# Kernel tuning notes

Measured on AMD Instinct MI355X. Metric: run time of the kernel, lower is better.

## Reference

```python
import jax, jax.numpy as jnp
import numpy as np

GAMMA = 0.96875


def setup_inputs() -> dict:
    key = jax.random.key(0)
    kx, kq, kk, kv = jax.random.split(key, 4)
    B, T, D = 4, 2048, 1024
    x = jax.random.normal(kx, (B, T, D), dtype=jnp.float32)
    Wq = jax.random.normal(kq, (D, D), dtype=jnp.float32) * (1.0 / np.sqrt(D))
    Wk = jax.random.normal(kk, (D, D), dtype=jnp.float32) * (1.0 / np.sqrt(D))
    Wv = jax.random.normal(kv, (D, D), dtype=jnp.float32) * (1.0 / np.sqrt(D))
    return {"x": x, "Wq": Wq, "Wk": Wk, "Wv": Wv}


def reference(x, Wq, Wk, Wv):
    # x: [B, T, D_in]; projections are bias-free Dense layers
    B, T, _ = x.shape
    D = Wq.shape[1]
    Q = jnp.einsum("bti,id->btd", x, Wq)  # [B,T,D]
    K = jnp.einsum("bti,id->btd", x, Wk)
    V = jnp.einsum("bti,id->btd", x, Wv)

    gamma = jnp.asarray(GAMMA, x.dtype)

    # Original: s[t] = gamma*s[t-1] + K[:,t,:]^T @ V[:,t,:]   (a [D,D] state,
    # batch is CONTRACTED by the matmul), then only reduce_sum over the last
    # state axis is used. The recurrence is linear, so it collapses exactly to
    # a [D]-vector recurrence with m_t[d] = sum_b K[b,t,d] * (sum_e V[b,t,e]).
    m = jnp.einsum("btd,bt->td", K, V.sum(axis=-1))  # [T,D]

    def step(s, mt):
        s_new = gamma * s + mt
        return s_new, s_new

    # loop runs t = 1..T-1 starting from s = 0; afterwards s[0] = s[1]
    _, states = jax.lax.scan(step, jnp.zeros((D,), x.dtype), m[1:])  # [T-1,D]
    S = jnp.concatenate([states[:1], states], axis=0)  # [T,D]

    # tf.reshape([T,D] -> [-1, T]) is a row-major element scramble, then transpose
    S = S.reshape(-1, T).T  # [T,D] (scrambled, faithful to the original)

    return S[None, :, :] * Q  # broadcast over batch -> [B,T,D]
```

## Files before the change

kernel.cpp:

```cpp
#include <hip/hip_runtime.h>
#include <hip/hip_bf16.h>
#include <cstddef>

#define T_DIM 2048
#define D_DIM 1024
#define GAMMA_F 0.96875f

typedef __attribute__((ext_vector_type(8))) short bf16x8;
typedef __attribute__((ext_vector_type(8))) ushort ushortx8;
typedef __attribute__((ext_vector_type(4))) float f32x4;

#define AS1 __attribute__((address_space(1)))
#define AS3 __attribute__((address_space(3)))

static __device__ inline ushort f2bs(float f) {
    __hip_bfloat16 h = __float2bfloat16(f);
    return *reinterpret_cast<ushort*>(&h);
}

constexpr float gpw(int n) {
    float r = 1.f;
    for (int i = 0; i < n; ++i) r *= GAMMA_F;
    return r;
}

template <int N>
static __device__ __forceinline__ void vm_wait() {
    static_assert(N == 0 || N == 2 || N == 3 || N == 4 || N == 6 || N == 8,
                  "vm_wait<N>: N not in emitted set");
    if constexpr (N == 0)      asm volatile("s_waitcnt vmcnt(0)" ::: "memory");
    else if constexpr (N == 2) asm volatile("s_waitcnt vmcnt(2)" ::: "memory");
    else if constexpr (N == 3) asm volatile("s_waitcnt vmcnt(3)" ::: "memory");
    else if constexpr (N == 4) asm volatile("s_waitcnt vmcnt(4)" ::: "memory");
    else if constexpr (N == 6) asm volatile("s_waitcnt vmcnt(6)" ::: "memory");
    else if constexpr (N == 8) asm volatile("s_waitcnt vmcnt(8)" ::: "memory");
}
static __device__ __forceinline__ void raw_barrier() {
    asm volatile("s_barrier" ::: "memory");
}
static __device__ __forceinline__ void lgkm0() {
    asm volatile("s_waitcnt lgkmcnt(0)" ::: "memory");
}

__global__ __launch_bounds__(256) void k_prep(const float* __restrict__ Wk,
                                              const float* __restrict__ Wq,
                                              const float* __restrict__ Wv,
                                              ushort* __restrict__ WTk,
                                              ushort* __restrict__ WTq,
                                              float* __restrict__ wv_sum) {
    const int tid = threadIdx.x;
    if (blockIdx.z == 2) {
        __shared__ float red[4];
        const int i = blockIdx.y * 32 + blockIdx.x;
        const float* row = Wv + (size_t)i * D_DIM;
        float p = 0.f;
        for (int c = tid; c < D_DIM; c += 256) p += row[c];
        for (int o = 32; o; o >>= 1) p += __shfl_down(p, o);
        if ((tid & 63) == 0) red[tid >> 6] = p;
        __syncthreads();
        if (tid == 0) wv_sum[i] = red[0] + red[1] + red[2] + red[3];
        return;
    }
    const float* W = (blockIdx.z == 0) ? Wk : Wq;
    ushort* WT     = (blockIdx.z == 0) ? WTk : WTq;
    __shared__ float tile[32][33];
    const int tx = tid & 31, ty = tid >> 5;
    const int kb = blockIdx.x * 32, nb = blockIdx.y * 32;
    #pragma unroll
    for (int r = 0; r < 4; ++r)
        tile[ty + 8 * r][tx] = W[(size_t)(kb + ty + 8 * r) * 1024 + nb + tx];
    __syncthreads();
    #pragma unroll
    for (int r = 0; r < 4; ++r)
        WT[(size_t)(nb + ty + 8 * r) * 1024 + kb + tx] =
            f2bs(tile[tx][ty + 8 * r]);
}

__global__ __launch_bounds__(256) void k_vsum_y(const float* __restrict__ x,
                                                const float* __restrict__ wv_sum,
                                                ushort* __restrict__ yb,
                                                ushort* __restrict__ xb) {
    __shared__ float xs[4][D_DIM];
    __shared__ float red[4][4];
    const int t = blockIdx.x;
    const int tid = threadIdx.x;
    const int lane = tid & 63, wv = tid >> 6;

    #pragma unroll
    for (int b = 0; b < 4; ++b) {
        const float4* xr = (const float4*)(x + ((size_t)b * T_DIM + t) * D_DIM);
        *(float4*)&xs[b][tid * 4] = xr[tid];
    }
    __syncthreads();

    #pragma unroll
    for (int b = 0; b < 4; ++b) {
        float p = 0.f;
        for (int c = tid; c < D_DIM; c += 256) p += xs[b][c] * wv_sum[c];
        for (int o = 32; o; o >>= 1) p += __shfl_down(p, o);
        if (lane == 0) red[wv][b] = p;
    }
    __syncthreads();

    float vs[4];
    #pragma unroll
    for (int b = 0; b < 4; ++b)
        vs[b] = red[0][b] + red[1][b] + red[2][b] + red[3][b];

    if (tid < 128) {
        const int i0 = tid * 8;
        ushortx8 yv;
        #pragma unroll
        for (int j = 0; j < 8; ++j) {
            float a = 0.f;
            #pragma unroll
            for (int b = 0; b < 4; ++b) a += xs[b][i0 + j] * vs[b];
            yv[j] = f2bs(a);
        }
        *(ushortx8*)(yb + (size_t)t * D_DIM + i0) = yv;
    }
    for (int g = tid; g < 512; g += 256) {
        const int b = g >> 7, i0 = (g & 127) * 8;
        ushortx8 xv;
        #pragma unroll
        for (int j = 0; j < 8; ++j) xv[j] = f2bs(xs[b][i0 + j]);
        *(ushortx8*)(xb + ((size_t)b * T_DIM + t) * D_DIM + i0) = xv;
    }
}

template <int MF, int NF, int MODE>
__global__ __launch_bounds__(512, 4) void k_gemm(const ushort* __restrict__ A,
                                                 const ushort* __restrict__ BT,
                                                 float* __restrict__ C,
                                                 const float* __restrict__ S2,
                                                 float* __restrict__ tot) {
    static_assert(MODE != 0 || MF == 2, "fused scan1 requires 32-row wave tiles");
    constexpr int BM = 4 * MF * 16;
    constexpr int BN = 2 * NF * 16;
    constexpr int LOADS = BM / 64 + BN / 64;
    __shared__ ushort As[2][BM][64];
    __shared__ ushort Bs[2][BN][64];
    const int tid = threadIdx.x;
    const int lane = tid & 63, wid = tid >> 6;
    const int wr = wid >> 1, wc = wid & 1;
    const int rowBase = blockIdx.x * BM;
    const int colBase = blockIdx.y * BN;

    f32x4 acc[MF][NF];
    #pragma unroll
    for (int i = 0; i < MF; ++i)
        #pragma unroll
        for (int j = 0; j < NF; ++j) acc[i][j] = f32x4{0.f, 0.f, 0.f, 0.f};

    auto stage = [&](int buf, int kb) {
        #pragma unroll
        for (int q = 0; q < BM / 64; ++q) {
            const int s = q * 8192 + tid * 16;
            const int r = s >> 7, grp = (s >> 4) & 7;
            const int gcol = kb + (((grp ^ (r & 7)) & 7) << 3);
            __builtin_amdgcn_global_load_lds(
                (const AS1 void*)(A + (size_t)(rowBase + r) * 1024 + gcol),
                (AS3 void*)((AS3 char*)&As[buf][0][0] + s), 16, 0, 0);
        }
        #pragma unroll
        for (int q = 0; q < BN / 64; ++q) {
            const int s = q * 8192 + tid * 16;
            const int r = s >> 7, grp = (s >> 4) & 7;
            const int gcol = kb + (((grp ^ (r & 7)) & 7) << 3);
            __builtin_amdgcn_global_load_lds(
                (const AS1 void*)(BT + (size_t)(colBase + r) * 1024 + gcol),
                (AS3 void*)((AS3 char*)&Bs[buf][0][0] + s), 16, 0, 0);
        }
    };

    stage(0, 0);

    #pragma unroll 2
    for (int kt = 0; kt < 16; ++kt) {
        const int cur = kt & 1;
        if (kt < 15) {
            stage(cur ^ 1, (kt + 1) * 64);
            vm_wait<LOADS>();
        } else {
            vm_wait<0>();
        }
        raw_barrier();

        bf16x8 af[2][MF], bfv[2][NF];
        #pragma unroll
        for (int ks = 0; ks < 2; ++ks) {
            const int kg = ks * 4 + (lane >> 4);
            #pragma unroll
            for (int mi = 0; mi < MF; ++mi) {
                const int r = wr * (MF * 16) + mi * 16 + (lane & 15);
                af[ks][mi] = *(const bf16x8*)((const char*)&As[cur][0][0] +
                                              r * 128 + (((kg ^ (r & 7)) & 7) << 4));
            }
            #pragma unroll
            for (int ni = 0; ni < NF; ++ni) {
                const int r = wc * (NF * 16) + ni * 16 + (lane & 15);
                bfv[ks][ni] = *(const bf16x8*)((const char*)&Bs[cur][0][0] +
                                               r * 128 + (((kg ^ (r & 7)) & 7) << 4));
            }
        }
        #pragma unroll
        for (int ks = 0; ks < 2; ++ks)
            #pragma unroll
            for (int mi = 0; mi < MF; ++mi)
                #pragma unroll
                for (int ni = 0; ni < NF; ++ni)
                    acc[mi][ni] = __builtin_amdgcn_mfma_f32_16x16x32_bf16(
                        af[ks][mi], bfv[ks][ni], acc[mi][ni], 0, 0, 0);

        lgkm0();
        raw_barrier();
    }

    #pragma unroll
    for (int mi = 0; mi < MF; ++mi) {
        #pragma unroll
        for (int ni = 0; ni < NF; ++ni) {
            const int col = colBase + wc * (NF * 16) + ni * 16 + (lane & 15);
            #pragma unroll
            for (int q = 0; q < 4; ++q) {
                const int row = rowBase + wr * (MF * 16) + mi * 16 + (lane >> 4) * 4 + q;
                float v = acc[mi][ni][q];
                if (MODE == 1)
                    v *= S2[(size_t)(row & (T_DIM - 1)) * D_DIM + col];
                C[(size_t)row * D_DIM + col] = v;
            }
        }
    }

    if (MODE == 0) {
        const int h = lane >> 4;
        const int t3 = 3 - h;
        const float A0 = ((t3 & 1) ? gpw(4) : 1.f) * ((t3 & 2) ? gpw(8) : 1.f);
        const int chunk = blockIdx.x * 4 + wr;
        #pragma unroll
        for (int ni = 0; ni < NF; ++ni) {
            float part = 0.f;
            #pragma unroll
            for (int mi = 0; mi < MF; ++mi)
                #pragma unroll
                for (int q = 0; q < 4; ++q)
                    part += (A0 * gpw(16 * (MF - 1 - mi) + (3 - q))) * acc[mi][ni][q];
            if (chunk == 0 && h == 0)
                part -= (A0 * gpw(16 * (MF - 1) + 3)) * acc[0][ni][0];
            part += __shfl_xor(part, 16);
            part += __shfl_xor(part, 32);
            if (h == 0) {
                const int col = colBase + wc * (NF * 16) + ni * 16 + (lane & 15);
                tot[(size_t)chunk * D_DIM + col] = part;
            }
        }
    }
}

#define SC_L 32
#define SC_NC 64

__global__ __launch_bounds__(256) void k_scan2(const float* __restrict__ m,
                                               const float* __restrict__ tot,
                                               float* __restrict__ S2) {
    __shared__ float ls[128][65];
    const int tid = threadIdx.x;
    const int cl = tid & 63;
    const int ch = tid >> 6;
    const int col = blockIdx.x * 64 + cl;
    const int chg = blockIdx.y * 4 + ch;
    const int t0 = chg * SC_L;

    constexpr float gL = gpw(SC_L);

    float carry = 0.f, f = 1.f;
    for (int j = chg - 1; j >= 0; --j) {
        carry += f * tot[(size_t)j * D_DIM + col];
        f *= gL;
    }

    float r = carry, s1 = 0.f;
    #pragma unroll 4
    for (int k = 0; k < SC_L; ++k) {
        const int t = t0 + k;
        const float a = (t == 0) ? 0.f : m[(size_t)t * D_DIM + col];
        r = GAMMA_F * r + a;
        ls[ch * SC_L + k][cl] = r;
        if (t == 1) s1 = r;
    }
    if (blockIdx.y == 0 && ch == 0) ls[0][cl] = s1;
    __syncthreads();

    const int c0 = blockIdx.x * 64;
    const int tB = blockIdx.y * 128;
    for (int e = tid; e < 128 * 64; e += 256) {
        const int rr = e >> 6;
        const int j  = e & 63;
        const int hi = rr >> 6, cl2 = rr & 63;
        S2[(size_t)((hi << 10) + c0 + cl2) * D_DIM + (tB >> 1) + j] =
            ls[2 * j + hi][cl2];
    }
}

extern "C" void kernel_launch(void* const* d_in, const int* in_sizes, int n_in,
                              void* d_out, int out_size, void* d_ws, size_t ws_size,
                              hipStream_t stream) {
    const float* x  = (const float*)d_in[0];
    const float* Wq = (const float*)d_in[1];
    const float* Wk = (const float*)d_in[2];
    const float* Wv = (const float*)d_in[3];
    float* out = (float*)d_out;
    char* ws = (char*)d_ws;

    ushort* xb  = (ushort*)(ws);
    float*  m   = (float*)(ws + (16u << 20));
    ushort* yb  = (ushort*)(ws + (24u << 20));
    ushort* WTk = (ushort*)(ws + (28u << 20));
    ushort* WTq = (ushort*)(ws + (30u << 20));
    float*  S2  = (float*)(ws + (32u << 20));
    float*  tot = (float*)(ws + (40u << 20));
    float*  wv_sum = m;

    dim3 gP(32, 32, 3);
    k_prep<<<gP, 256, 0, stream>>>(Wk, Wq, Wv, WTk, WTq, wv_sum);

    k_vsum_y<<<T_DIM, 256, 0, stream>>>(x, wv_sum, (ushort*)yb, (ushort*)xb);

    dim3 gm(T_DIM / 128, D_DIM / 64);
    k_gemm<2, 2, 0><<<gm, 512, 0, stream>>>(yb, WTk, m, nullptr, tot);

    dim3 gs(D_DIM / 64, SC_NC / 4);
    k_scan2<<<gs, 256, 0, stream>>>(m, tot, S2);

    dim3 gq((4 * T_DIM) / 128, D_DIM / 128);
    k_gemm<2, 4, 1><<<gq, 512, 0, stream>>>(xb, WTq, out, S2, nullptr);
}
```

Measured before the change: 78.02 us.

## Fuse K-gemm, scan and Q-gemm into one persistent kernel with atomic semaphores

After: 123.1 us. +57.8%, slower.

```diff
diff --git a/kernel.cpp b/kernel.cpp
--- a/kernel.cpp
+++ b/kernel.cpp
@@ -40,6 +40,22 @@
 }
 static __device__ __forceinline__ void lgkm0() {
     asm volatile("s_waitcnt lgkmcnt(0)" ::: "memory");
+}
+
+static __device__ __forceinline__ void sem_signal(unsigned* sem) {
+    __syncthreads();
+    if (threadIdx.x == 0) {
+        __threadfence();
+        atomicAdd(sem, 1u);
+    }
+}
+static __device__ __forceinline__ void sem_wait(unsigned* sem, unsigned target) {
+    if (threadIdx.x == 0) {
+        while (__hip_atomic_load(sem, __ATOMIC_RELAXED, __HIP_MEMORY_SCOPE_AGENT) < target)
+            __builtin_amdgcn_s_sleep(16);
+        __threadfence();
+    }
+    __syncthreads();
 }
 
 __global__ __launch_bounds__(256) void k_prep(const float* __restrict__ Wk,
@@ -129,7 +145,8 @@
 }
 
 template <int MF, int NF, int MODE>
-__global__ __launch_bounds__(512, 4) void k_gemm(const ushort* __restrict__ A,
+static __device__ __forceinline__ void gemm_body(char* smem, int bx, int by,
+                                                 const ushort* __restrict__ A,
                                                  const ushort* __restrict__ BT,
                                                  float* __restrict__ C,
                                                  const float* __restrict__ S2,
@@ -138,13 +155,14 @@
     constexpr int BM = 4 * MF * 16;
     constexpr int BN = 2 * NF * 16;
     constexpr int LOADS = BM / 64 + BN / 64;
-    __shared__ ushort As[2][BM][64];
-    __shared__ ushort Bs[2][BN][64];
+    constexpr int ABYTES = BM * 128;
+    constexpr int AOFF2  = 2 * ABYTES;
+    constexpr int BBYTES = BN * 128;
     const int tid = threadIdx.x;
     const int lane = tid & 63, wid = tid >> 6;
     const int wr = wid >> 1, wc = wid & 1;
-    const int rowBase = blockIdx.x * BM;
-    const int colBase = blockIdx.y * BN;
+    const int rowBase = bx * BM;
+    const int colBase = by * BN;
 
     f32x4 acc[MF][NF];
     #pragma unroll
@@ -160,7 +178,7 @@
             const int gcol = kb + (((grp ^ (r & 7)) & 7) << 3);
             __builtin_amdgcn_global_load_lds(
                 (const AS1 void*)(A + (size_t)(rowBase + r) * 1024 + gcol),
-                (AS3 void*)((AS3 char*)&As[buf][0][0] + s), 16, 0, 0);
+                (AS3 void*)((AS3 char*)smem + buf * ABYTES + s), 16, 0, 0);
         }
         #pragma unroll
         for (int q = 0; q < BN / 64; ++q) {
@@ -169,7 +187,7 @@
             const int gcol = kb + (((grp ^ (r & 7)) & 7) << 3);
             __builtin_amdgcn_global_load_lds(
                 (const AS1 void*)(BT + (size_t)(colBase + r) * 1024 + gcol),
-                (AS3 void*)((AS3 char*)&Bs[buf][0][0] + s), 16, 0, 0);
+                (AS3 void*)((AS3 char*)smem + AOFF2 + buf * BBYTES + s), 16, 0, 0);
         }
     };
 
@@ -193,13 +211,13 @@
             #pragma unroll
             for (int mi = 0; mi < MF; ++mi) {
                 const int r = wr * (MF * 16) + mi * 16 + (lane & 15);
-                af[ks][mi] = *(const bf16x8*)((const char*)&As[cur][0][0] +
+                af[ks][mi] = *(const bf16x8*)(smem + cur * ABYTES +
                                               r * 128 + (((kg ^ (r & 7)) & 7) << 4));
             }
             #pragma unroll
             for (int ni = 0; ni < NF; ++ni) {
                 const int r = wc * (NF * 16) + ni * 16 + (lane & 15);
-                bfv[ks][ni] = *(const bf16x8*)((const char*)&Bs[cur][0][0] +
+                bfv[ks][ni] = *(const bf16x8*)(smem + AOFF2 + cur * BBYTES +
                                                r * 128 + (((kg ^ (r & 7)) & 7) << 4));
             }
         }
@@ -236,7 +254,7 @@
         const int h = lane >> 4;
         const int t3 = 3 - h;
         const float A0 = ((t3 & 1) ? gpw(4) : 1.f) * ((t3 & 2) ? gpw(8) : 1.f);
-        const int chunk = blockIdx.x * 4 + wr;
+        const int chunk = bx * 4 + wr;
         #pragma unroll
         for (int ni = 0; ni < NF; ++ni) {
             float part = 0.f;
@@ -258,48 +276,74 @@
 }
 
 #define SC_L 32
-#define SC_NC 64
-
-__global__ __launch_bounds__(256) void k_scan2(const float* __restrict__ m,
-                                               const float* __restrict__ tot,
-                                               float* __restrict__ S2) {
-    __shared__ float ls[128][65];
+
+static __device__ __forceinline__ void scan2_body(char* smem, int bx, int by,
+                                                  const float* __restrict__ m,
+                                                  const float* __restrict__ tot,
+                                                  float* __restrict__ S2) {
+    float (*ls)[65] = (float(*)[65])smem;
     const int tid = threadIdx.x;
-    const int cl = tid & 63;
-    const int ch = tid >> 6;
-    const int col = blockIdx.x * 64 + cl;
-    const int chg = blockIdx.y * 4 + ch;
-    const int t0 = chg * SC_L;
-
-    constexpr float gL = gpw(SC_L);
-
-    float carry = 0.f, f = 1.f;
-    for (int j = chg - 1; j >= 0; --j) {
-        carry += f * tot[(size_t)j * D_DIM + col];
-        f *= gL;
-    }
-
-    float r = carry, s1 = 0.f;
-    #pragma unroll 4
-    for (int k = 0; k < SC_L; ++k) {
-        const int t = t0 + k;
-        const float a = (t == 0) ? 0.f : m[(size_t)t * D_DIM + col];
-        r = GAMMA_F * r + a;
-        ls[ch * SC_L + k][cl] = r;
-        if (t == 1) s1 = r;
-    }
-    if (blockIdx.y == 0 && ch == 0) ls[0][cl] = s1;
-    __syncthreads();
-
-    const int c0 = blockIdx.x * 64;
-    const int tB = blockIdx.y * 128;
-    for (int e = tid; e < 128 * 64; e += 256) {
+    if (tid < 256) {
+        const int cl = tid & 63;
+        const int ch = tid >> 6;
+        const int col = bx * 64 + cl;
+        const int chg = by * 4 + ch;
+        const int t0 = chg * SC_L;
+
+        constexpr float gL = gpw(SC_L);
+        float carry = 0.f, f = 1.f;
+        for (int j = chg - 1; j >= 0; --j) {
+            carry += f * tot[(size_t)j * D_DIM + col];
+            f *= gL;
+        }
+
+        float r = carry, s1 = 0.f;
+        #pragma unroll 4
+        for (int k = 0; k < SC_L; ++k) {
+            const int t = t0 + k;
+            const float a = (t == 0) ? 0.f : m[(size_t)t * D_DIM + col];
+            r = GAMMA_F * r + a;
+            ls[ch * SC_L + k][cl] = r;
+            if (t == 1) s1 = r;
+        }
+        if (by == 0 && ch == 0) ls[0][cl] = s1;
+    }
+    __syncthreads();
+
+    const int c0 = bx * 64;
+    const int tB = by * 128;
+    for (int e = tid; e < 128 * 64; e += 512) {
         const int rr = e >> 6;
         const int j  = e & 63;
         const int hi = rr >> 6, cl2 = rr & 63;
         S2[(size_t)((hi << 10) + c0 + cl2) * D_DIM + (tB >> 1) + j] =
             ls[2 * j + hi][cl2];
     }
+    __syncthreads();
+}
+
+__global__ __launch_bounds__(512, 4) void k_mega(const ushort* yb,
+                                                 const ushort* WTk,
+                                                 float* m, float* tot,
+                                                 float* S2,
+                                                 const ushort* xb,
+                                                 const ushort* WTq,
+                                                 float* out,
+                                                 unsigned* sem) {
+    __shared__ char smem[65536];
+    const int b = blockIdx.x;
+    unsigned* semA = sem;
+    unsigned* semB = sem + 32;
+
+    if (b < 256) {
+        gemm_body<2, 2, 0>(smem, b & 15, b >> 4, yb, WTk, m, nullptr, tot);
+        sem_signal(semA);
+        sem_wait(semA, 256);
+        scan2_body(smem, b & 15, b >> 4, m, tot, S2);
+        sem_signal(semB);
+    }
+    sem_wait(semB, 256);
+    gemm_body<2, 4, 1>(smem, b & 63, b >> 6, xb, WTq, out, S2, nullptr);
 }
 
 extern "C" void kernel_launch(void* const* d_in, const int* in_sizes, int n_in,
@@ -319,6 +363,7 @@
     ushort* WTq = (ushort*)(ws + (30u << 20));
     float*  S2  = (float*)(ws + (32u << 20));
     float*  tot = (float*)(ws + (40u << 20));
+    unsigned* sem = (unsigned*)(ws + (40u << 20) + (512u << 10));
     float*  wv_sum = m;
 
     dim3 gP(32, 32, 3);
@@ -326,12 +371,7 @@
 
     k_vsum_y<<<T_DIM, 256, 0, stream>>>(x, wv_sum, (ushort*)yb, (ushort*)xb);
 
-    dim3 gm(T_DIM / 128, D_DIM / 64);
-    k_gemm<2, 2, 0><<<gm, 512, 0, stream>>>(yb, WTk, m, nullptr, tot);
-
-    dim3 gs(D_DIM / 64, SC_NC / 4);
-    k_scan2<<<gs, 256, 0, stream>>>(m, tot, S2);
-
-    dim3 gq((4 * T_DIM) / 128, D_DIM / 128);
-    k_gemm<2, 4, 1><<<gq, 512, 0, stream>>>(xb, WTq, out, S2, nullptr);
-}
+    hipMemsetAsync(sem, 0, 256, stream);
+
+    k_mega<<<512, 512, 0, stream>>>(yb, WTk, m, tot, S2, xb, WTq, out, sem);
+}
```
